# Kernel tuning notes

Measured on AMD Instinct MI355X. Metric: run time of the kernel, lower is better.

## Reference

```python
import jax, jax.numpy as jnp
import numpy as np


def setup_inputs() -> dict:
    key = jax.random.key(0)
    k1, k2 = jax.random.split(key)
    B, N, F, K = 8, 8192, 128, 512
    x = jax.random.normal(k1, (B, N, F), dtype=jnp.float32)
    cluster_centers = jax.random.normal(k2, (K, F), dtype=jnp.float32)
    return {"x": x, "cluster_centers": cluster_centers}


def reference(x, cluster_centers):
    # same math as sqrt(sum((x - c)^2)) without the [B,N,K,F] intermediate).
    x_sq = jnp.sum(x * x, axis=-1, keepdims=True)                 # [B, N, 1]
    c_sq = jnp.sum(cluster_centers * cluster_centers, axis=-1)    # [K]
    cross = jnp.einsum("bnf,kf->bnk", x, cluster_centers)         # [B, N, K]
    d2 = jnp.maximum(x_sq + c_sq[None, None, :] - 2.0 * cross, 0.0)
    distances = jnp.sqrt(d2)                                      # [B, N, K]
    associations = jax.nn.softmax(-distances, axis=-1)            # [B, N, K]
    output = jnp.einsum("bnk,kf->bnf", associations, cluster_centers)
    return output
```

## Files before the change

kernel.cpp:

```cpp
#include <hip/hip_runtime.h>
#include <hip/hip_bf16.h>

typedef short v8s __attribute__((ext_vector_type(8)));
typedef float v16f __attribute__((ext_vector_type(16)));
typedef unsigned v2u __attribute__((ext_vector_type(2)));

#define F_ 128
#define K_ 512
#define M_ 65536
#define CH_SH 17408
#define CB_OFF 9216

__device__ __forceinline__ short f2bf(float f) {
    union { float f; unsigned u; } v; v.f = f;
    unsigned u = v.u;
    u = (u + 0x7FFFu + ((u >> 16) & 1u)) >> 16;
    return (short)u;
}
__device__ __forceinline__ float bf2f(short s) {
    union { float f; unsigned u; } v;
    v.u = ((unsigned)(unsigned short)s) << 16;
    return v.f;
}

#if __has_builtin(__builtin_amdgcn_permlane32_swap)
#define HAVE_PLS 1
#endif

__device__ __forceinline__ void pswap(unsigned &a, unsigned &b, int lane) {
#ifdef HAVE_PLS
    v2u r = __builtin_amdgcn_permlane32_swap(a, b, false, false);
    a = (unsigned)r.x; b = (unsigned)r.y;
#else
    unsigned sa = (unsigned)__shfl_xor((int)a, 32);
    unsigned sb = (unsigned)__shfl_xor((int)b, 32);
    if (lane & 32) a = sb; else b = sa;
#endif
}

__global__ void prep_kernel(const float* __restrict__ centers, short* __restrict__ G) {
    const int c = blockIdx.x;
    const int f = threadIdx.x;
    const int ch = c >> 6, c64 = c & 63;
    const size_t base = (size_t)ch * CH_SH;
    float v = centers[c * F_ + f];
    short b = f2bf(v);
    float vb = bf2f(b);
    { const int ks = f >> 4, h = (f >> 3) & 1, j = f & 7;
      G[base + (size_t)((ks * 2 + h) * 64 + c64) * 8 + j] = b; }
    { const int kap = c64 >> 4, hh = (c64 >> 3) & 1, jj = c64 & 7;
      G[base + CB_OFF + (size_t)((kap * 2 + hh) * F_ + f) * 8 + jj] = b; }
    float s = vb * vb;
    #pragma unroll
    for (int off = 1; off < 64; off <<= 1) s += __shfl_xor(s, off);
    __shared__ float part[2];
    if ((f & 63) == 0) part[f >> 6] = s;
    __syncthreads();
    if (f < 16) {
        const float csq = part[0] + part[1];
        const float chv = -0.5f * csq;
        const short vh = f2bf(chv);
        const short vl = f2bf(chv - bf2f(vh));
        const short val = (f == 0) ? vh : (f == 1) ? vl : (f == 2) ? (short)0x3F80 : (short)0;
        const int h2 = f >> 3, j2 = f & 7;
        G[base + (size_t)((16 + h2) * 64 + c64) * 8 + j2] = val;
    }
}

__device__ __forceinline__ void stage1(const short* __restrict__ CbS, const v8s* Bx,
                                       v16f& a0, v16f& a1, int h, int c32) {
    #pragma unroll
    for (int e2 = 0; e2 < 16; ++e2) { a0[e2] = 0.f; a1[e2] = 0.f; }
    v8s f0a = *(const v8s*)&CbS[(size_t)((0 * 2 + h) * 64 + c32) * 8];
    v8s f1a = *(const v8s*)&CbS[(size_t)((0 * 2 + h) * 64 + 32 + c32) * 8];
    v8s f0b = *(const v8s*)&CbS[(size_t)((1 * 2 + h) * 64 + c32) * 8];
    v8s f1b = *(const v8s*)&CbS[(size_t)((1 * 2 + h) * 64 + 32 + c32) * 8];
    #pragma unroll
    for (int ks = 0; ks < 9; ++ks) {
        v8s c0 = f0a, c1 = f1a;
        f0a = f0b; f1a = f1b;
        if (ks < 7) {
            f0b = *(const v8s*)&CbS[(size_t)(((ks + 2) * 2 + h) * 64 + c32) * 8];
            f1b = *(const v8s*)&CbS[(size_t)(((ks + 2) * 2 + h) * 64 + 32 + c32) * 8];
        }
        a0 = __builtin_amdgcn_mfma_f32_32x32x16_bf16(c0, Bx[ks], a0, 0, 0, 0);
        a1 = __builtin_amdgcn_mfma_f32_32x32x16_bf16(c1, Bx[ks], a1, 0, 0, 0);
    }
}

__device__ __forceinline__ void epi_ct(const v16f acc, const short* __restrict__ CTS, int ct,
                                       float& lden, v16f (&Of)[4], int h, int c32, int lane) {
    v8s cf[8];
    #pragma unroll
    for (int kp = 0; kp < 2; ++kp)
        #pragma unroll
        for (int ft = 0; ft < 4; ++ft)
            cf[kp * 4 + ft] = *(const v8s*)
                &CTS[(size_t)(((ct * 2 + kp) * 2 + h) * F_ + ft * 32 + c32) * 8];
    unsigned U[8];
    #pragma unroll
    for (int t = 0; t < 8; ++t) {
        const float d20 = fmaxf(-2.0f * acc[2 * t], 0.f);
        const float d21 = fmaxf(-2.0f * acc[2 * t + 1], 0.f);
        const float p0 = __expf(-__builtin_amdgcn_sqrtf(d20));
        const float p1 = __expf(-__builtin_amdgcn_sqrtf(d21));
        union { __hip_bfloat162 hh; unsigned u; } cv;
        cv.hh = __float22bfloat162_rn(make_float2(p0, p1));
        U[t] = cv.u;
        lden += __uint_as_float(cv.u << 16);
        lden += __uint_as_float(cv.u & 0xffff0000u);
    }
    #pragma unroll
    for (int kp = 0; kp < 2; ++kp) {
        unsigned s0 = U[4 * kp],     s2 = U[4 * kp + 2];
        unsigned s1 = U[4 * kp + 1], s3 = U[4 * kp + 3];
        pswap(s0, s2, lane);
        pswap(s1, s3, lane);
        union { v8s v; unsigned u[4]; } pf;
        pf.u[0] = s0; pf.u[1] = s1; pf.u[2] = s2; pf.u[3] = s3;
        #pragma unroll
        for (int ft = 0; ft < 4; ++ft)
            Of[ft] = __builtin_amdgcn_mfma_f32_32x32x16_bf16(pf.v, cf[kp * 4 + ft], Of[ft], 0, 0, 0);
    }
}

__global__ __launch_bounds__(512, 2) void cluster_kernel(
        const float* __restrict__ x, const short* __restrict__ G,
        float* __restrict__ out) {
    __shared__ float MB[4][65][64];
    const int tid = threadIdx.x;
    const int wave = tid >> 6, lane = tid & 63;
    const int s = wave & 1, p = wave >> 1;
    const int h = lane >> 5, c32 = lane & 31;
    const int row0 = blockIdx.x * 128 + p * 32;
    const int off = blockIdx.x & 7;

    const float4* xr4 = (const float4*)(x + (size_t)(row0 + c32) * F_);
    float4 xl[16];
    #pragma unroll
    for (int ks = 0; ks < 8; ++ks) {
        xl[2 * ks]     = xr4[ks * 4 + h * 2];
        xl[2 * ks + 1] = xr4[ks * 4 + h * 2 + 1];
    }
    v8s Bx[9];
    float xs = 0.f;
    #pragma unroll
    for (int ks = 0; ks < 8; ++ks) {
        float vv[8] = {xl[2*ks].x, xl[2*ks].y, xl[2*ks].z, xl[2*ks].w,
                       xl[2*ks+1].x, xl[2*ks+1].y, xl[2*ks+1].z, xl[2*ks+1].w};
        v8s fr;
        #pragma unroll
        for (int j = 0; j < 8; ++j) {
            short bb = f2bf(vv[j]);
            fr[j] = bb;
            float r = bf2f(bb);
            xs += r * r;
        }
        Bx[ks] = fr;
    }
    xs += __shfl_xor(xs, 32);
    {
        const float xh = -0.5f * xs;
        const short sxh = f2bf(xh);
        const short sxl = f2bf(xh - bf2f(sxh));
        v8s e = (v8s){0, 0, 0, 0, 0, 0, 0, 0};
        if (h == 0) { e[0] = (short)0x3F80; e[1] = (short)0x3F80; e[2] = sxh; e[3] = sxl; }
        Bx[8] = e;
    }

    v16f Of[4];
    #pragma unroll
    for (int ft = 0; ft < 4; ++ft)
        #pragma unroll
        for (int e2 = 0; e2 < 16; ++e2) Of[ft][e2] = 0.f;
    float lden = 0.f;

    #pragma unroll 1
    for (int j = 0; j < 4; ++j) {
        const int ch = (off + s * 4 + j) & 7;
        const short* Cb = G + (size_t)ch * CH_SH;
        v16f a0, a1;
        stage1(Cb, Bx, a0, a1, h, c32);
        epi_ct(a0, Cb + CB_OFF, 0, lden, Of, h, c32, lane);
        epi_ct(a1, Cb + CB_OFF, 1, lden, Of, h, c32, lane);
    }

    if (s == 1) {
        #pragma unroll
        for (int ft = 0; ft < 4; ++ft)
            #pragma unroll
            for (int e2 = 0; e2 < 16; ++e2)
                MB[p][ft * 16 + e2][lane] = Of[ft][e2];
        MB[p][64][lane] = lden;
    }
    __syncthreads();
    if (s == 1) return;
    #pragma unroll
    for (int ft = 0; ft < 4; ++ft)
        #pragma unroll
        for (int e2 = 0; e2 < 16; ++e2)
            Of[ft][e2] += MB[p][ft * 16 + e2][lane];
    lden += MB[p][64][lane];

    lden += __shfl_xor(lden, 32);
    const float inv = 1.0f / lden;
    float invr[16];
    #pragma unroll
    for (int r = 0; r < 16; ++r)
        invr[r] = __shfl(inv, (r & 3) + 8 * (r >> 2) + 4 * h);
    #pragma unroll
    for (int ft = 0; ft < 4; ++ft)
        #pragma unroll
        for (int r = 0; r < 16; ++r) {
            const int xrow = (r & 3) + 8 * (r >> 2) + 4 * h;
            out[(size_t)(row0 + xrow) * F_ + ft * 32 + c32] = Of[ft][r] * invr[r];
        }
}

extern "C" void kernel_launch(void* const* d_in, const int* in_sizes, int n_in,
                              void* d_out, int out_size, void* d_ws, size_t ws_size,
                              hipStream_t stream) {
    const float* x       = (const float*)d_in[0];
    const float* centers = (const float*)d_in[1];
    float* out = (float*)d_out;
    short* G = (short*)d_ws;
    prep_kernel<<<K_, F_, 0, stream>>>(centers, G);
    cluster_kernel<<<M_ / 128, 512, 0, stream>>>(x, G, out);
}
```

Measured before the change: 111.2 us.

## Software-pipeline distance GEMM of next chunk with epilogue of previous chunk

Restructures the per-chunk loop so the first GEMM (distances) for chunk j is issued before the softmax/second-GEMM epilogue of chunk j-1, letting MFMA work overlap the exp/sqrt and global loads. It also deepens the center-fragment prefetch in stage1 from two to three stages. This keeps two extra 16-float accumulator sets live, which raises VGPR pressure under launch_bounds(512,2) and risks spills or lower occupancy.

```diff
diff --git a/kernel.cpp b/kernel.cpp
--- a/kernel.cpp
+++ b/kernel.cpp
@@ -67,21 +67,22 @@
     }
 }
 
-__device__ __forceinline__ void stage1(const short* __restrict__ CbS, const v8s* Bx,
-                                       v16f& a0, v16f& a1, int h, int c32) {
+__device__ __forceinline__ void stage1_d3(const short* __restrict__ Cb, const v8s* Bx,
+                                          v16f& a0, v16f& a1, int h, int c32) {
     #pragma unroll
     for (int e2 = 0; e2 < 16; ++e2) { a0[e2] = 0.f; a1[e2] = 0.f; }
-    v8s f0a = *(const v8s*)&CbS[(size_t)((0 * 2 + h) * 64 + c32) * 8];
-    v8s f1a = *(const v8s*)&CbS[(size_t)((0 * 2 + h) * 64 + 32 + c32) * 8];
-    v8s f0b = *(const v8s*)&CbS[(size_t)((1 * 2 + h) * 64 + c32) * 8];
-    v8s f1b = *(const v8s*)&CbS[(size_t)((1 * 2 + h) * 64 + 32 + c32) * 8];
+    v8s w0[3], w1[3];
+    #pragma unroll
+    for (int i = 0; i < 3; ++i) {
+        w0[i] = *(const v8s*)&Cb[(size_t)((i * 2 + h) * 64 + c32) * 8];
+        w1[i] = *(const v8s*)&Cb[(size_t)((i * 2 + h) * 64 + 32 + c32) * 8];
+    }
     #pragma unroll
     for (int ks = 0; ks < 9; ++ks) {
-        v8s c0 = f0a, c1 = f1a;
-        f0a = f0b; f1a = f1b;
-        if (ks < 7) {
-            f0b = *(const v8s*)&CbS[(size_t)(((ks + 2) * 2 + h) * 64 + c32) * 8];
-            f1b = *(const v8s*)&CbS[(size_t)(((ks + 2) * 2 + h) * 64 + 32 + c32) * 8];
+        v8s c0 = w0[ks % 3], c1 = w1[ks % 3];
+        if (ks < 6) {
+            w0[ks % 3] = *(const v8s*)&Cb[(size_t)(((ks + 3) * 2 + h) * 64 + c32) * 8];
+            w1[ks % 3] = *(const v8s*)&Cb[(size_t)(((ks + 3) * 2 + h) * 64 + 32 + c32) * 8];
         }
         a0 = __builtin_amdgcn_mfma_f32_32x32x16_bf16(c0, Bx[ks], a0, 0, 0, 0);
         a1 = __builtin_amdgcn_mfma_f32_32x32x16_bf16(c1, Bx[ks], a1, 0, 0, 0);
@@ -175,15 +176,26 @@
         for (int e2 = 0; e2 < 16; ++e2) Of[ft][e2] = 0.f;
     float lden = 0.f;
 
+    v16f a0p, a1p;
+    const short* prevCT;
+    {
+        const short* Cb = G + (size_t)((off + s * 4) & 7) * CH_SH;
+        stage1_d3(Cb, Bx, a0p, a1p, h, c32);
+        prevCT = Cb + CB_OFF;
+    }
+
     #pragma unroll 1
-    for (int j = 0; j < 4; ++j) {
-        const int ch = (off + s * 4 + j) & 7;
-        const short* Cb = G + (size_t)ch * CH_SH;
+    for (int j = 1; j < 4; ++j) {
+        const short* Cb = G + (size_t)((off + s * 4 + j) & 7) * CH_SH;
         v16f a0, a1;
-        stage1(Cb, Bx, a0, a1, h, c32);
-        epi_ct(a0, Cb + CB_OFF, 0, lden, Of, h, c32, lane);
-        epi_ct(a1, Cb + CB_OFF, 1, lden, Of, h, c32, lane);
-    }
+        stage1_d3(Cb, Bx, a0, a1, h, c32);
+        epi_ct(a0p, prevCT, 0, lden, Of, h, c32, lane);
+        epi_ct(a1p, prevCT, 1, lden, Of, h, c32, lane);
+        a0p = a0; a1p = a1;
+        prevCT = Cb + CB_OFF;
+    }
+    epi_ct(a0p, prevCT, 0, lden, Of, h, c32, lane);
+    epi_ct(a1p, prevCT, 1, lden, Of, h, c32, lane);
 
     if (s == 1) {
         #pragma unroll
```

Measured after the change: 146.3 us. 31.6% more time.
